# Optimization experiments

Hardware: AMD Instinct MI355X
Metric: run time of the kernel (lower is better)

Reference implementation:

```python
import jax, jax.numpy as jnp
import numpy as np

NEG_SLOPE = 0.01  # torch leaky_relu default

N_NODES = 100000
N_EDGES = 1600000
D = 64
N_BBOX = 4096


def setup_inputs() -> dict:
    key = jax.random.key(0)
    ks = jax.random.split(key, 9)
    x = jax.random.normal(ks[0], (N_NODES, D), dtype=jnp.float32)
    edge_index = jax.random.randint(ks[1], (2, N_EDGES), 0, N_NODES, dtype=jnp.int64)
    bbox = jax.random.randint(ks[2], (N_BBOX,), 0, N_NODES, dtype=jnp.int64)
    s = 1.0 / np.sqrt(D)
    W1_rel = jax.random.normal(ks[3], (D, D), dtype=jnp.float32) * s
    b1 = jax.random.normal(ks[4], (D,), dtype=jnp.float32) * s
    W1_root = jax.random.normal(ks[5], (D, D), dtype=jnp.float32) * s
    W2_rel = jax.random.normal(ks[6], (D, D), dtype=jnp.float32) * s
    b2 = jax.random.normal(ks[7], (D,), dtype=jnp.float32) * s
    W2_root = jax.random.normal(ks[8], (D, D), dtype=jnp.float32) * s
    return {"x": x, "edge_index": edge_index, "bbox": bbox,
            "W1_rel": W1_rel, "b1": b1, "W1_root": W1_root,
            "W2_rel": W2_rel, "b2": b2, "W2_root": W2_root}


def graph_conv(x, src, dst, W_rel, b, W_root):
    # PyG GraphConv: out_i = W_rel @ (sum_{j in N(i)} x_j) + b + W_root @ x_i
    msg = x[src]                                        # [E, D] gather
    agg = jax.ops.segment_sum(msg, dst, num_segments=x.shape[0])  # [N, D] scatter-add
    return agg @ W_rel + b + x @ W_root


def reference(x, edge_index, bbox, W1_rel, b1, W1_root, W2_rel, b2, W2_root):
    src, dst = edge_index[0], edge_index[1]
    h = graph_conv(x, src, dst, W1_rel, b1, W1_root)
    h = jax.nn.leaky_relu(h, NEG_SLOPE)
    # dropout is identity at inference (training=False)
    h = graph_conv(h, src, dst, W2_rel, b2, W2_root)
    h = jax.nn.leaky_relu(h, NEG_SLOPE)
    return h[bbox]
```

## Files before the change

kernel.cpp:

```cpp
#include <hip/hip_runtime.h>

#define N_NODES 100000
#define N_EDGES 1600000
#define D 64
#define N_BBOX 4096
#define CAP 64
#define NBITW 3136
#define SLICE 12500
#define NBLK_A 6250
#define SEGCAP 64

typedef short bf16x8 __attribute__((ext_vector_type(8)));
typedef float f32x4 __attribute__((ext_vector_type(4)));

__device__ __forceinline__ float readlane_f(float v, int l) {
  return __int_as_float(__builtin_amdgcn_readlane(__float_as_int(v), l));
}
__device__ __forceinline__ int bperm(int srclane, int v) {
  return __builtin_amdgcn_ds_bpermute(srclane << 2, v);
}
__device__ __forceinline__ float lrelu(float v) {
  return fmaxf(v, 0.01f * v);
}
__device__ __forceinline__ bool testbit(const unsigned* bits, int i) {
  return (bits[i >> 5] >> (i & 31)) & 1u;
}
__device__ __forceinline__ short f2bf(float f) {
  unsigned u = __float_as_uint(f);
  u += 0x7FFFu + ((u >> 16) & 1u);
  return (short)(u >> 16);
}
__device__ __forceinline__ float bf2f(short s) {
  return __uint_as_float(((unsigned)(unsigned short)s) << 16);
}

__global__ __launch_bounds__(256) void mark_kernel(const int* __restrict__ bbox,
                                                   unsigned* __restrict__ is_bbox_bits,
                                                   unsigned* __restrict__ needed_bits) {
  int t = blockIdx.x * blockDim.x + threadIdx.x;
  if (t < N_BBOX) {
    int n = bbox[t];
    unsigned m = 1u << (n & 31);
    atomicOr(&is_bbox_bits[n >> 5], m);
    atomicOr(&needed_bits[n >> 5], m);
  }
}

__global__ __launch_bounds__(256) void mark_needed_kernel(
    const int* __restrict__ src, const int* __restrict__ dst,
    const unsigned* __restrict__ is_bbox_bits, unsigned* __restrict__ needed_bits) {
  int e = blockIdx.x * blockDim.x + threadIdx.x;
  if (e >= N_EDGES) return;
  int d = dst[e];
  if (testbit(is_bbox_bits, d)) {
    int s = src[e];
    atomicOr(&needed_bits[s >> 5], 1u << (s & 31));
  }
}

__global__ __launch_bounds__(256) void binA_kernel(const int* __restrict__ src,
                                                   const int* __restrict__ dst,
                                                   const unsigned* __restrict__ needed_bits,
                                                   int* __restrict__ qcnt,
                                                   int* __restrict__ qseg) {
  __shared__ int lcnt[8];
  __shared__ int lbuf[8 * SEGCAP];
  const int t = threadIdx.x;
  const int e = blockIdx.x * 256 + t;
  if (t < 8) lcnt[t] = 0;
  __syncthreads();

  const int d = dst[e];
  if (testbit(needed_bits, d)) {
    const int q = d / SLICE;
    const int p = atomicAdd(&lcnt[q], 1);
    if (p < SEGCAP) lbuf[q * SEGCAP + p] = src[e] | ((d - q * SLICE) << 17);
  }
  __syncthreads();

  const size_t segbase = (size_t)blockIdx.x * 8;
  if (t < 8) qcnt[segbase + t] = (lcnt[t] > SEGCAP) ? SEGCAP : lcnt[t];
  for (int i = t; i < 8 * SEGCAP; i += 256) {
    const int q = i >> 6, p = i & 63;
    if (p < lcnt[q]) qseg[(segbase + q) * SEGCAP + p] = lbuf[i];
  }
}

__global__ __launch_bounds__(256) void scatterB_kernel(const int* __restrict__ qcnt,
                                                       const int* __restrict__ qseg,
                                                       int* __restrict__ cnt,
                                                       int* __restrict__ slots) {
  const int sl = blockIdx.x & 7;
  const int bidx = blockIdx.x >> 3;
  const int nblk = gridDim.x >> 3;
  const int base_node = sl * SLICE;
  const int sub = threadIdx.x >> 4;
  const int pp = threadIdx.x & 15;

  for (int b0 = bidx * 16; b0 < NBLK_A; b0 += nblk * 16) {
    const int b = b0 + sub;
    if (b >= NBLK_A) continue;
    const int n = qcnt[(size_t)b * 8 + sl];
    const int* seg = qseg + ((size_t)b * 8 + sl) * SEGCAP;
    for (int p = pp; p < n; p += 16) {
      const int pv = seg[p];
      const int d = base_node + (pv >> 17);
      const int pos = atomicAdd(&cnt[d], 1);
      if (pos < CAP) slots[(size_t)d * CAP + pos] = pv & 0x1FFFF;
    }
  }
}

__global__ __launch_bounds__(256) void xprep_kernel(const float4* __restrict__ x4,
                                                    bf16x8* __restrict__ xb) {
  int i = blockIdx.x * blockDim.x + threadIdx.x;
  if (i < N_NODES * 8) {
    const float4 a = x4[i * 2], b = x4[i * 2 + 1];
    bf16x8 r;
    r[0] = f2bf(a.x); r[1] = f2bf(a.y); r[2] = f2bf(a.z); r[3] = f2bf(a.w);
    r[4] = f2bf(b.x); r[5] = f2bf(b.y); r[6] = f2bf(b.z); r[7] = f2bf(b.w);
    xb[i] = r;
  }
}

__global__ __launch_bounds__(256) void gather1_kernel(const uint4* __restrict__ xb,
                                                      const unsigned* __restrict__ needed_bits,
                                                      const int* __restrict__ cnt,
                                                      const int* __restrict__ slots,
                                                      bf16x8* __restrict__ aggb) {
  const int wid = (blockIdx.x * blockDim.x + threadIdx.x) >> 6;
  if (wid >= N_NODES) return;
  if (!testbit(needed_bits, wid)) return;
  const int lane = threadIdx.x & 63;
  const int g = lane >> 3, c = lane & 7;

  int n = cnt[wid];
  n = (n > CAP) ? CAP : n;
  const int myslot = (lane < n) ? slots[(size_t)wid * CAP + lane] : 0;

  float accf[8] = {0.f, 0.f, 0.f, 0.f, 0.f, 0.f, 0.f, 0.f};
  for (int e0 = 0; e0 < n; e0 += 64) {
    int idx[8], s[8];
    uint4 v[8];
#pragma unroll
    for (int u = 0; u < 8; u++) {
      idx[u] = e0 + u * 8 + g;
      s[u] = bperm(idx[u], myslot);
    }
#pragma unroll
    for (int u = 0; u < 8; u++) {
      v[u] = make_uint4(0u, 0u, 0u, 0u);
      if (idx[u] < n) v[u] = xb[(size_t)s[u] * 8 + c];
    }
#pragma unroll
    for (int u = 0; u < 8; u++) {
      accf[0] += __uint_as_float(v[u].x << 16);
      accf[1] += __uint_as_float(v[u].x & 0xFFFF0000u);
      accf[2] += __uint_as_float(v[u].y << 16);
      accf[3] += __uint_as_float(v[u].y & 0xFFFF0000u);
      accf[4] += __uint_as_float(v[u].z << 16);
      accf[5] += __uint_as_float(v[u].z & 0xFFFF0000u);
      accf[6] += __uint_as_float(v[u].w << 16);
      accf[7] += __uint_as_float(v[u].w & 0xFFFF0000u);
    }
  }
#pragma unroll
  for (int off = 8; off < 64; off <<= 1)
#pragma unroll
    for (int i = 0; i < 8; i++) accf[i] += __shfl_xor(accf[i], off);

  if (lane < 8) {
    bf16x8 r;
#pragma unroll
    for (int i = 0; i < 8; i++) r[i] = f2bf(accf[i]);
    aggb[(size_t)wid * 8 + lane] = r;
  }
}

__global__ __launch_bounds__(256, 1) void dense1_mfma_kernel(
    const short* __restrict__ xb, const short* __restrict__ aggb,
    const float* __restrict__ W1rel, const float* __restrict__ b1,
    const float* __restrict__ W1root, short* __restrict__ hb) {
  const int lane = threadIdx.x & 63;
  const int cn = lane & 15;
  const int quad = lane >> 4;
  const int wid0 = (blockIdx.x * blockDim.x + threadIdx.x) >> 6;
  const int nwaves = (gridDim.x * blockDim.x) >> 6;

  bf16x8 brel[2][4], broot[2][4];
#pragma unroll
  for (int kh = 0; kh < 2; kh++)
#pragma unroll
    for (int nt = 0; nt < 4; nt++)
#pragma unroll
      for (int i = 0; i < 8; i++) {
        const int k = kh * 32 + quad * 8 + i;
        brel[kh][nt][i] = f2bf(W1rel[k * D + nt * 16 + cn]);
        broot[kh][nt][i] = f2bf(W1root[k * D + nt * 16 + cn]);
      }
  float bj[4];
#pragma unroll
  for (int nt = 0; nt < 4; nt++) bj[nt] = b1[nt * 16 + cn];

  for (int tile = wid0; tile < N_NODES / 16; tile += nwaves) {
    const int node0 = tile * 16;
    const short* arow = aggb + (size_t)(node0 + cn) * D;
    const short* xrow = xb + (size_t)(node0 + cn) * D;

    f32x4 acc[4] = {};
#pragma unroll
    for (int kh = 0; kh < 2; kh++) {
      const int kb = kh * 32 + quad * 8;
      const bf16x8 a_agg = *(const bf16x8*)(arow + kb);
      const bf16x8 a_x = *(const bf16x8*)(xrow + kb);
#pragma unroll
      for (int nt = 0; nt < 4; nt++) {
        acc[nt] = __builtin_amdgcn_mfma_f32_16x16x32_bf16(a_agg, brel[kh][nt],
                                                          acc[nt], 0, 0, 0);
        acc[nt] = __builtin_amdgcn_mfma_f32_16x16x32_bf16(a_x, broot[kh][nt],
                                                          acc[nt], 0, 0, 0);
      }
    }
#pragma unroll
    for (int nt = 0; nt < 4; nt++) {
#pragma unroll
      for (int r = 0; r < 4; r++) {
        const int row = quad * 4 + r;
        hb[(size_t)(node0 + row) * D + nt * 16 + cn] = f2bf(lrelu(acc[nt][r] + bj[nt]));
      }
    }
  }
}

__global__ __launch_bounds__(256, 1) void layer2_kernel(
    const uint4* __restrict__ hb4, const int* __restrict__ cnt,
    const int* __restrict__ slots, const int* __restrict__ bbox,
    const float* __restrict__ W2rel, const float* __restrict__ b2,
    const float* __restrict__ W2root, float* __restrict__ out) {
  const int t = (blockIdx.x * blockDim.x + threadIdx.x) >> 6;
  if (t >= N_BBOX) return;
  const int lane = threadIdx.x & 63;
  const int g = lane >> 3, c = lane & 7;

  float wrel[D], wroot[D];
#pragma unroll
  for (int k = 0; k < D; k++) {
    wrel[k] = W2rel[k * D + lane];
    wroot[k] = W2root[k * D + lane];
  }
  const float bj = b2[lane];

  const int node = __builtin_amdgcn_readfirstlane(bbox[t]);
  int n = cnt[node];
  n = (n > CAP) ? CAP : n;
  const int myslot = (lane < n) ? slots[(size_t)node * CAP + lane] : 0;

  float accf[8] = {0.f, 0.f, 0.f, 0.f, 0.f, 0.f, 0.f, 0.f};
  for (int e0 = 0; e0 < n; e0 += 64) {
    int idx[8], s[8];
    uint4 v[8];
#pragma unroll
    for (int u = 0; u < 8; u++) {
      idx[u] = e0 + u * 8 + g;
      s[u] = bperm(idx[u], myslot);
    }
#pragma unroll
    for (int u = 0; u < 8; u++) {
      v[u] = make_uint4(0u, 0u, 0u, 0u);
      if (idx[u] < n) v[u] = hb4[(size_t)s[u] * 8 + c];
    }
#pragma unroll
    for (int u = 0; u < 8; u++) {
      accf[0] += __uint_as_float(v[u].x << 16);
      accf[1] += __uint_as_float(v[u].x & 0xFFFF0000u);
      accf[2] += __uint_as_float(v[u].y << 16);
      accf[3] += __uint_as_float(v[u].y & 0xFFFF0000u);
      accf[4] += __uint_as_float(v[u].z << 16);
      accf[5] += __uint_as_float(v[u].z & 0xFFFF0000u);
      accf[6] += __uint_as_float(v[u].w << 16);
      accf[7] += __uint_as_float(v[u].w & 0xFFFF0000u);
    }
  }
#pragma unroll
  for (int off = 8; off < 64; off <<= 1)
#pragma unroll
    for (int i = 0; i < 8; i++) accf[i] += __shfl_xor(accf[i], off);

  const float hi = bf2f(((const short*)hb4)[(size_t)node * D + lane]);
  float s0 = 0.f, s1 = 0.f, s2 = 0.f, s3 = 0.f;
#pragma unroll
  for (int k = 0; k < D; k += 2) {
    const float a0 = readlane_f(accf[k & 7], k >> 3);
    const float a1 = readlane_f(accf[(k + 1) & 7], (k + 1) >> 3);
    s0 += a0 * wrel[k];
    s1 += readlane_f(hi, k) * wroot[k];
    s2 += a1 * wrel[k + 1];
    s3 += readlane_f(hi, k + 1) * wroot[k + 1];
  }
  out[(size_t)t * D + lane] = lrelu(bj + ((s0 + s1) + (s2 + s3)));
}


extern "C" void kernel_launch(void* const* d_in, const int* in_sizes, int n_in,
                              void* d_out, int out_size, void* d_ws, size_t ws_size,
                              hipStream_t stream) {
  const float* x = (const float*)d_in[0];
  const int* ei = (const int*)d_in[1];
  const int* src = ei;
  const int* dst = ei + N_EDGES;
  const int* bbox = (const int*)d_in[2];
  const float* W1rel = (const float*)d_in[3];
  const float* b1 = (const float*)d_in[4];
  const float* W1root = (const float*)d_in[5];
  const float* W2rel = (const float*)d_in[6];
  const float* b2 = (const float*)d_in[7];
  const float* W2root = (const float*)d_in[8];
  float* out = (float*)d_out;

  char* ws = (char*)d_ws;
  size_t off = 0;
  auto alloc = [&](size_t bytes) -> char* {
    char* p = ws + off;
    off = (off + bytes + 511) & ~(size_t)511;
    return p;
  };
  unsigned* is_bbox_bits = (unsigned*)alloc(NBITW * sizeof(unsigned));
  unsigned* needed_bits = (unsigned*)alloc(NBITW * sizeof(unsigned));
  int* cnt = (int*)alloc(N_NODES * sizeof(int));
  char* zero_end = ws + off;
  int* qcnt = (int*)alloc((size_t)NBLK_A * 8 * sizeof(int));
  int* slots = (int*)alloc((size_t)N_NODES * CAP * sizeof(int));
  short* xb = (short*)alloc((size_t)N_NODES * D * sizeof(short));
  short* aggb = (short*)alloc((size_t)N_NODES * D * sizeof(short));
  char* ovl = alloc((size_t)N_NODES * D * sizeof(short));
  int* qseg = (int*)ovl;
  short* hb = (short*)ovl;

  hipMemsetAsync(is_bbox_bits, 0, (size_t)(zero_end - (char*)is_bbox_bits), stream);
  mark_kernel<<<(N_BBOX + 255) / 256, 256, 0, stream>>>(bbox, is_bbox_bits,
                                                        needed_bits);
  mark_needed_kernel<<<(N_EDGES + 255) / 256, 256, 0, stream>>>(
      src, dst, is_bbox_bits, needed_bits);
  binA_kernel<<<NBLK_A, 256, 0, stream>>>(src, dst, needed_bits, qcnt, qseg);
  xprep_kernel<<<(N_NODES * 8 + 255) / 256, 256, 0, stream>>>((const float4*)x,
                                                              (bf16x8*)xb);
  scatterB_kernel<<<1024, 256, 0, stream>>>(qcnt, qseg, cnt, slots);
  gather1_kernel<<<(N_NODES + 3) / 4, 256, 0, stream>>>(
      (const uint4*)xb, needed_bits, cnt, slots, (bf16x8*)aggb);
  dense1_mfma_kernel<<<512, 256, 0, stream>>>(xb, aggb, W1rel, b1, W1root, hb);
  layer2_kernel<<<(N_BBOX + 3) / 4, 256, 0, stream>>>(
      (const uint4*)hb, cnt, slots, bbox, W2rel, b2, W2root, out);
}
```

Before: 199.4 us.

## Fuse edge marking with binning and merge bbox marking into bf16 conversion

```diff
diff --git a/kernel.cpp b/kernel.cpp
--- a/kernel.cpp
+++ b/kernel.cpp
@@ -8,7 +8,7 @@
 #define NBITW 3136
 #define SLICE 12500
 #define NBLK_A 6250
-#define SEGCAP 64
+#define SEGCAP 96
 
 typedef short bf16x8 __attribute__((ext_vector_type(8)));
 typedef float f32x4 __attribute__((ext_vector_type(4)));
@@ -34,33 +34,33 @@
   return __uint_as_float(((unsigned)(unsigned short)s) << 16);
 }
 
-__global__ __launch_bounds__(256) void mark_kernel(const int* __restrict__ bbox,
+__global__ __launch_bounds__(256) void prep_kernel(const float4* __restrict__ x4,
+                                                   bf16x8* __restrict__ xb,
+                                                   const int* __restrict__ bbox,
                                                    unsigned* __restrict__ is_bbox_bits,
                                                    unsigned* __restrict__ needed_bits) {
-  int t = blockIdx.x * blockDim.x + threadIdx.x;
-  if (t < N_BBOX) {
-    int n = bbox[t];
-    unsigned m = 1u << (n & 31);
-    atomicOr(&is_bbox_bits[n >> 5], m);
-    atomicOr(&needed_bits[n >> 5], m);
-  }
-}
-
-__global__ __launch_bounds__(256) void mark_needed_kernel(
-    const int* __restrict__ src, const int* __restrict__ dst,
-    const unsigned* __restrict__ is_bbox_bits, unsigned* __restrict__ needed_bits) {
-  int e = blockIdx.x * blockDim.x + threadIdx.x;
-  if (e >= N_EDGES) return;
-  int d = dst[e];
-  if (testbit(is_bbox_bits, d)) {
-    int s = src[e];
-    atomicOr(&needed_bits[s >> 5], 1u << (s & 31));
-  }
-}
-
-__global__ __launch_bounds__(256) void binA_kernel(const int* __restrict__ src,
+  const int i = blockIdx.x * 256 + threadIdx.x;
+  if (i < N_NODES * 8) {
+    const float4 a = x4[i * 2], b = x4[i * 2 + 1];
+    bf16x8 r;
+    r[0] = f2bf(a.x); r[1] = f2bf(a.y); r[2] = f2bf(a.z); r[3] = f2bf(a.w);
+    r[4] = f2bf(b.x); r[5] = f2bf(b.y); r[6] = f2bf(b.z); r[7] = f2bf(b.w);
+    xb[i] = r;
+  } else {
+    const int t = i - N_NODES * 8;
+    if (t < N_BBOX) {
+      const int n = bbox[t];
+      const unsigned m = 1u << (n & 31);
+      atomicOr(&is_bbox_bits[n >> 5], m);
+      atomicOr(&needed_bits[n >> 5], m);
+    }
+  }
+}
+
+__global__ __launch_bounds__(256) void scan_kernel(const int* __restrict__ src,
                                                    const int* __restrict__ dst,
-                                                   const unsigned* __restrict__ needed_bits,
+                                                   const unsigned* __restrict__ is_bbox_bits,
+                                                   unsigned* __restrict__ needed_bits,
                                                    int* __restrict__ qcnt,
                                                    int* __restrict__ qseg) {
   __shared__ int lcnt[8];
@@ -71,23 +71,26 @@
   __syncthreads();
 
   const int d = dst[e];
-  if (testbit(needed_bits, d)) {
-    const int q = d / SLICE;
-    const int p = atomicAdd(&lcnt[q], 1);
-    if (p < SEGCAP) lbuf[q * SEGCAP + p] = src[e] | ((d - q * SLICE) << 17);
-  }
+  const int s = src[e];
+  if (testbit(is_bbox_bits, d)) {
+    atomicOr(&needed_bits[s >> 5], 1u << (s & 31));
+  }
+  const int q = d / SLICE;
+  const int p = atomicAdd(&lcnt[q], 1);
+  if (p < SEGCAP) lbuf[q * SEGCAP + p] = s | ((d - q * SLICE) << 17);
   __syncthreads();
 
   const size_t segbase = (size_t)blockIdx.x * 8;
   if (t < 8) qcnt[segbase + t] = (lcnt[t] > SEGCAP) ? SEGCAP : lcnt[t];
   for (int i = t; i < 8 * SEGCAP; i += 256) {
-    const int q = i >> 6, p = i & 63;
-    if (p < lcnt[q]) qseg[(segbase + q) * SEGCAP + p] = lbuf[i];
+    const int q2 = i / SEGCAP, p2 = i - q2 * SEGCAP;
+    if (p2 < lcnt[q2]) qseg[(segbase + q2) * SEGCAP + p2] = lbuf[i];
   }
 }
 
 __global__ __launch_bounds__(256) void scatterB_kernel(const int* __restrict__ qcnt,
                                                        const int* __restrict__ qseg,
+                                                       const unsigned* __restrict__ needed_bits,
                                                        int* __restrict__ cnt,
                                                        int* __restrict__ slots) {
   const int sl = blockIdx.x & 7;
@@ -105,21 +108,10 @@
     for (int p = pp; p < n; p += 16) {
       const int pv = seg[p];
       const int d = base_node + (pv >> 17);
+      if (!testbit(needed_bits, d)) continue;
       const int pos = atomicAdd(&cnt[d], 1);
       if (pos < CAP) slots[(size_t)d * CAP + pos] = pv & 0x1FFFF;
     }
-  }
-}
-
-__global__ __launch_bounds__(256) void xprep_kernel(const float4* __restrict__ x4,
-                                                    bf16x8* __restrict__ xb) {
-  int i = blockIdx.x * blockDim.x + threadIdx.x;
-  if (i < N_NODES * 8) {
-    const float4 a = x4[i * 2], b = x4[i * 2 + 1];
-    bf16x8 r;
-    r[0] = f2bf(a.x); r[1] = f2bf(a.y); r[2] = f2bf(a.z); r[3] = f2bf(a.w);
-    r[4] = f2bf(b.x); r[5] = f2bf(b.y); r[6] = f2bf(b.z); r[7] = f2bf(b.w);
-    xb[i] = r;
   }
 }
 
@@ -329,22 +321,18 @@
   int* cnt = (int*)alloc(N_NODES * sizeof(int));
   char* zero_end = ws + off;
   int* qcnt = (int*)alloc((size_t)NBLK_A * 8 * sizeof(int));
+  int* qseg = (int*)alloc((size_t)NBLK_A * 8 * SEGCAP * sizeof(int));
   int* slots = (int*)alloc((size_t)N_NODES * CAP * sizeof(int));
   short* xb = (short*)alloc((size_t)N_NODES * D * sizeof(short));
   short* aggb = (short*)alloc((size_t)N_NODES * D * sizeof(short));
-  char* ovl = alloc((size_t)N_NODES * D * sizeof(short));
-  int* qseg = (int*)ovl;
-  short* hb = (short*)ovl;
+  short* hb = (short*)alloc((size_t)N_NODES * D * sizeof(short));
 
   hipMemsetAsync(is_bbox_bits, 0, (size_t)(zero_end - (char*)is_bbox_bits), stream);
-  mark_kernel<<<(N_BBOX + 255) / 256, 256, 0, stream>>>(bbox, is_bbox_bits,
-                                                        needed_bits);
-  mark_needed_kernel<<<(N_EDGES + 255) / 256, 256, 0, stream>>>(
-      src, dst, is_bbox_bits, needed_bits);
-  binA_kernel<<<NBLK_A, 256, 0, stream>>>(src, dst, needed_bits, qcnt, qseg);
-  xprep_kernel<<<(N_NODES * 8 + 255) / 256, 256, 0, stream>>>((const float4*)x,
-                                                              (bf16x8*)xb);
-  scatterB_kernel<<<1024, 256, 0, stream>>>(qcnt, qseg, cnt, slots);
+  prep_kernel<<<(N_NODES * 8 + N_BBOX + 255) / 256, 256, 0, stream>>>(
+      (const float4*)x, (bf16x8*)xb, bbox, is_bbox_bits, needed_bits);
+  scan_kernel<<<NBLK_A, 256, 0, stream>>>(src, dst, is_bbox_bits, needed_bits,
+                                          qcnt, qseg);
+  scatterB_kernel<<<1024, 256, 0, stream>>>(qcnt, qseg, needed_bits, cnt, slots);
   gather1_kernel<<<(N_NODES + 3) / 4, 256, 0, stream>>>(
       (const uint4*)xb, needed_bits, cnt, slots, (bf16x8*)aggb);
   dense1_mfma_kernel<<<512, 256, 0, stream>>>(xb, aggb, W1rel, b1, W1root, hb);
```

Measured after the change: 193.6 us. 2.9% less time.
